# Kernel tuning notes

Hardware: AMD Instinct MI355X
Metric: run time of the kernel (lower is better)

Reference implementation:

```python
import jax, jax.numpy as jnp
import numpy as np

N = 100000
E = 2000000
K = 3


def setup_inputs() -> dict:
    key = jax.random.key(0)
    ks = jax.random.split(key, 6)
    x = jax.random.normal(ks[0], (N, 1), jnp.float32)
    edge_index = jax.random.randint(ks[1], (2, E), 0, N, dtype=jnp.int64)
    W1 = jax.random.normal(ks[2], (K, 1, 32), jnp.float32) * 0.5
    b1 = jnp.zeros((32,), jnp.float32)
    W2 = jax.random.normal(ks[3], (K, 32, 32), jnp.float32) * (1.0 / np.sqrt(32.0))
    b2 = jnp.zeros((32,), jnp.float32)
    Wfc = jax.random.normal(ks[4], (32, 1), jnp.float32) * (1.0 / np.sqrt(32.0))
    bfc = jnp.zeros((1,), jnp.float32)
    return dict(x=x, edge_index=edge_index, W1=W1, b1=b1, W2=W2, b2=b2, Wfc=Wfc, bfc=bfc)


def _cheb_norm(edge_index, n):
    # PyG ChebConv.__norm__ with normalization='sym', lambda_max=2.0:
    # L = I - D^{-1/2} A D^{-1/2}; L_hat = (2/lmax)*L - I = -D^{-1/2} A D^{-1/2} (zero diag)
    src, dst = edge_index[0], edge_index[1]
    w = jnp.ones((edge_index.shape[1],), jnp.float32)
    deg = jax.ops.segment_sum(w, src, num_segments=n)
    dinv = jnp.where(deg > 0, jax.lax.rsqrt(jnp.maximum(deg, 1.0)), 0.0)
    norm = -dinv[src] * w * dinv[dst]
    return src, dst, norm


def _propagate(x, src, dst, norm, n):
    # y[i] = sum_{e: dst[e]=i} norm[e] * x[src[e]]  (gather-scatter SpMM)
    return jax.ops.segment_sum(norm[:, None] * x[src], dst, num_segments=n)


def _cheb_conv(x, src, dst, norm, W, b, n):
    Tx0 = x
    out = Tx0 @ W[0]
    Tx1 = _propagate(Tx0, src, dst, norm, n)
    out = out + Tx1 @ W[1]
    for k in range(2, W.shape[0]):  # small fixed K, structurally distinct weights
        Tx2 = 2.0 * _propagate(Tx1, src, dst, norm, n) - Tx0
        out = out + Tx2 @ W[k]
        Tx0, Tx1 = Tx1, Tx2
    return out + b


def reference(x, edge_index, W1, b1, W2, b2, Wfc, bfc):
    n = x.shape[0]
    src, dst, norm = _cheb_norm(edge_index, n)
    h = jax.nn.relu(_cheb_conv(x, src, dst, norm, W1, b1, n))
    h = jax.nn.relu(_cheb_conv(h, src, dst, norm, W2, b2, n))
    return h @ Wfc + bfc
```

## Files before the change

### kernel.cpp

```cpp
#include <hip/hip_runtime.h>
#include <hip/hip_fp16.h>


#define BS 256
#define NC 32
#define NRH 16
#define NRB 16
#define HB 1024
#define RCAP 6250

__global__ __launch_bounds__(HB) void k_hist32(const int* __restrict__ src,
                                               const int* __restrict__ dst,
                                               int* __restrict__ deg32,
                                               int* __restrict__ cnt32,
                                               int n, int E, int ce) {
    __shared__ int hcnt[RCAP];
    __shared__ int hdeg[RCAP];
    int b = blockIdx.x, c = b & (NC - 1), r = b >> 5;
    int t = threadIdx.x;
    const int R = (n + NRH - 1) / NRH;
    int lo = r * R, hi = min(lo + R, n), len = hi - lo;
    for (int q = t; q < len; q += HB) { hcnt[q] = 0; hdeg[q] = 0; }
    __syncthreads();
    int e0 = c * ce, e1 = min(e0 + ce, E);
    if (e0 < e1) {
        const int4* d4 = reinterpret_cast<const int4*>(dst + e0);
        const int4* s4 = reinterpret_cast<const int4*>(src + e0);
        int L4 = (e1 - e0) >> 2;
        for (int m = 0; m * 4 * HB < L4; ++m) {
            int4 dv[4], sv[4];
            bool ok[4];
            #pragma unroll
            for (int q = 0; q < 4; ++q) {
                int idx = t + (m * 4 + q) * HB;
                ok[q] = idx < L4;
                if (ok[q]) { dv[q] = d4[idx]; sv[q] = s4[idx]; }
            }
            #pragma unroll
            for (int q = 0; q < 4; ++q) if (ok[q]) {
                int d;
                d = dv[q].x; if (d >= lo && d < hi) atomicAdd(&hcnt[d - lo], 1);
                d = dv[q].y; if (d >= lo && d < hi) atomicAdd(&hcnt[d - lo], 1);
                d = dv[q].z; if (d >= lo && d < hi) atomicAdd(&hcnt[d - lo], 1);
                d = dv[q].w; if (d >= lo && d < hi) atomicAdd(&hcnt[d - lo], 1);
                d = sv[q].x; if (d >= lo && d < hi) atomicAdd(&hdeg[d - lo], 1);
                d = sv[q].y; if (d >= lo && d < hi) atomicAdd(&hdeg[d - lo], 1);
                d = sv[q].z; if (d >= lo && d < hi) atomicAdd(&hdeg[d - lo], 1);
                d = sv[q].w; if (d >= lo && d < hi) atomicAdd(&hdeg[d - lo], 1);
            }
        }
        for (int e = e0 + ((e1 - e0) & ~3) + t; e < e1; e += HB) {
            int d = dst[e];
            if (d >= lo && d < hi) atomicAdd(&hcnt[d - lo], 1);
            int s = src[e];
            if (s >= lo && s < hi) atomicAdd(&hdeg[s - lo], 1);
        }
    }
    __syncthreads();
    int base = c * n + lo;
    for (int q = t; q < len; q += HB) {
        cnt32[base + q] = hcnt[q];
        deg32[base + q] = hdeg[q];
    }
}

__global__ void k_dinv32(const int* __restrict__ deg32, const int* __restrict__ cnt32,
                         const float* __restrict__ x, float* __restrict__ dinv,
                         float* __restrict__ u, float* __restrict__ w,
                         int* __restrict__ cnt, int n) {
    int i = blockIdx.x * BS + threadIdx.x;
    if (i < n) {
        int d = 0, ci = 0;
        #pragma unroll
        for (int c = 0; c < NC; ++c) { d += deg32[c * n + i]; ci += cnt32[c * n + i]; }
        float df = (float)d;
        float dv = (d > 0) ? rsqrtf(fmaxf(df, 1.0f)) : 0.0f;
        dinv[i] = dv;
        u[i] = dv * x[i];
        w[i] = -dv * dv;
        cnt[i] = ci;
    }
}

__global__ void k_scan2A(const int* __restrict__ cnt, int* __restrict__ rowptr,
                         int* __restrict__ part, int n) {
    __shared__ int sh[BS];
    int t = threadIdx.x, i = blockIdx.x * BS + t;
    int v = (i < n) ? cnt[i] : 0;
    sh[t] = v; __syncthreads();
    int acc = v;
    for (int d = 1; d < BS; d <<= 1) {
        int add = (t >= d) ? sh[t - d] : 0;
        __syncthreads();
        acc += add; sh[t] = acc;
        __syncthreads();
    }
    if (i < n) rowptr[i] = acc - v;
    if (t == BS - 1) part[blockIdx.x] = acc;
}

__global__ void k_scanB(int* __restrict__ part, int nb) {
    __shared__ int sh[512];
    int t = threadIdx.x;
    int v = (t < nb) ? part[t] : 0;
    sh[t] = v; __syncthreads();
    int acc = v;
    for (int d = 1; d < 512; d <<= 1) {
        int add = (t >= d) ? sh[t - d] : 0;
        __syncthreads();
        acc += add; sh[t] = acc;
        __syncthreads();
    }
    if (t < nb) part[t] = acc - v;
}

__global__ void k_scan2C(int* __restrict__ rowptr, const int* __restrict__ part, int n, int E) {
    int i = blockIdx.x * BS + threadIdx.x;
    if (i < n) rowptr[i] += part[i >> 8];
    if (i == n) rowptr[n] = E;
}

__global__ void k_frag(const int* __restrict__ cnt32, const int* __restrict__ rowptr,
                       int* __restrict__ cur32, int n) {
    int i = blockIdx.x * BS + threadIdx.x;
    if (i < n) {
        int run = rowptr[i];
        #pragma unroll
        for (int c = 0; c < NC; ++c) {
            cur32[c * n + i] = run;
            run += cnt32[c * n + i];
        }
    }
}

__global__ __launch_bounds__(HB) void k_build32(const int* __restrict__ src,
                                                const int* __restrict__ dst,
                                                const int* __restrict__ cur32,
                                                int* __restrict__ colv,
                                                int n, int E, int ce) {
    __shared__ int lcur[RCAP];
    int b = blockIdx.x, r = b & (NRB - 1), c = b >> 4;
    int t = threadIdx.x;
    const int R = (n + NRB - 1) / NRB;
    int lo = r * R, hi = min(lo + R, n), len = hi - lo;
    int base = c * n + lo;
    for (int q = t; q < len; q += HB) lcur[q] = cur32[base + q];
    __syncthreads();
    int e0 = c * ce, e1 = min(e0 + ce, E);
    if (e0 < e1) {
        const int4* d4 = reinterpret_cast<const int4*>(dst + e0);
        const int4* s4 = reinterpret_cast<const int4*>(src + e0);
        int L4 = (e1 - e0) >> 2;
        for (int m = 0; m * 4 * HB < L4; ++m) {
            int4 dv[4], sv[4];
            bool ok[4];
            #pragma unroll
            for (int q = 0; q < 4; ++q) {
                int idx = t + (m * 4 + q) * HB;
                ok[q] = idx < L4;
                if (ok[q]) { dv[q] = d4[idx]; sv[q] = s4[idx]; }
            }
            #pragma unroll
            for (int q = 0; q < 4; ++q) if (ok[q]) {
                int d;
                d = dv[q].x; if (d >= lo && d < hi) { int p = atomicAdd(&lcur[d - lo], 1); colv[p] = sv[q].x; }
                d = dv[q].y; if (d >= lo && d < hi) { int p = atomicAdd(&lcur[d - lo], 1); colv[p] = sv[q].y; }
                d = dv[q].z; if (d >= lo && d < hi) { int p = atomicAdd(&lcur[d - lo], 1); colv[p] = sv[q].z; }
                d = dv[q].w; if (d >= lo && d < hi) { int p = atomicAdd(&lcur[d - lo], 1); colv[p] = sv[q].w; }
            }
        }
        for (int e = e0 + ((e1 - e0) & ~3) + t; e < e1; e += HB) {
            int d = dst[e];
            if (d >= lo && d < hi) { int p = atomicAdd(&lcur[d - lo], 1); colv[p] = src[e]; }
        }
    }
}

__global__ void k_prop_s(const int* __restrict__ rowptr, const int* __restrict__ colv,
                         const float* __restrict__ in, float* __restrict__ g,
                         float* __restrict__ vout, const float* __restrict__ w, int n) {
    int i = blockIdx.x * BS + threadIdx.x;
    if (i >= n) return;
    int b = rowptr[i], e = rowptr[i + 1];
    float s = 0.0f;
    int j = b;
    for (; j + 4 <= e; j += 4) {
        int s0 = colv[j], s1 = colv[j + 1], s2 = colv[j + 2], s3 = colv[j + 3];
        float a0 = in[s0], a1 = in[s1], a2 = in[s2], a3 = in[s3];
        s += (a0 + a1) + (a2 + a3);
    }
    for (; j < e; ++j) s += in[colv[j]];
    g[i] = s;
    if (vout) vout[i] = w[i] * s;
}

__global__ void k_layer1(const float* __restrict__ x, const float* __restrict__ g1,
                         const float* __restrict__ g2, const float* __restrict__ dinv,
                         const float* __restrict__ W1, const float* __restrict__ b1,
                         float* __restrict__ h, __half* __restrict__ hs16, int n) {
    int idx = blockIdx.x * BS + threadIdx.x;
    if (idx < n * 32) {
        int i = idx >> 5, f = idx & 31;
        float x0 = x[i], dv = dinv[i];
        float t1 = -dv * g1[i];
        float t2 = -2.0f * dv * g2[i] - x0;
        float v = x0 * W1[f] + t1 * W1[32 + f] + t2 * W1[64 + f] + b1[f];
        v = fmaxf(v, 0.0f);
        h[idx] = v;
        hs16[idx] = __float2half_rn(dv * v);
    }
}

__global__ void k_prop_vh(const int* __restrict__ rowptr, const int* __restrict__ colv,
                          const __half* __restrict__ in16, float* __restrict__ outf,
                          __half* __restrict__ out16, int n) {
    int t = blockIdx.x * BS + threadIdx.x;
    int node = t >> 3;
    if (node >= n) return;
    int ln4 = (t & 7) << 2;
    int b = rowptr[node], e = rowptr[node + 1];
    float4 acc = make_float4(0.f, 0.f, 0.f, 0.f);
    int j = b;
    for (; j + 8 <= e; j += 8) {
        int sx[8];
        #pragma unroll
        for (int q = 0; q < 8; ++q) sx[q] = colv[j + q];
        float2 raw[8];
        #pragma unroll
        for (int q = 0; q < 8; ++q)
            raw[q] = *reinterpret_cast<const float2*>(in16 + (size_t)sx[q] * 32 + ln4);
        #pragma unroll
        for (int q = 0; q < 8; ++q) {
            __half2 p0 = *reinterpret_cast<__half2*>(&raw[q].x);
            __half2 p1 = *reinterpret_cast<__half2*>(&raw[q].y);
            float2 a = __half22float2(p0), c = __half22float2(p1);
            acc.x += a.x; acc.y += a.y; acc.z += c.x; acc.w += c.y;
        }
    }
    for (; j < e; ++j) {
        int s = colv[j];
        float2 raw = *reinterpret_cast<const float2*>(in16 + (size_t)s * 32 + ln4);
        __half2 p0 = *reinterpret_cast<__half2*>(&raw.x);
        __half2 p1 = *reinterpret_cast<__half2*>(&raw.y);
        float2 a = __half22float2(p0), c = __half22float2(p1);
        acc.x += a.x; acc.y += a.y; acc.z += c.x; acc.w += c.y;
    }
    *reinterpret_cast<float4*>(outf + (size_t)node * 32 + ln4) = acc;
    __half2 o0 = __floats2half2_rn(acc.x, acc.y);
    __half2 o1 = __floats2half2_rn(acc.z, acc.w);
    float2 packed;
    *reinterpret_cast<__half2*>(&packed.x) = o0;
    *reinterpret_cast<__half2*>(&packed.y) = o1;
    *reinterpret_cast<float2*>(out16 + (size_t)node * 32 + ln4) = packed;
}

__global__ __launch_bounds__(BS) void k_prop_fc(
    const int* __restrict__ rowptr, const int* __restrict__ colv,
    const __half* __restrict__ gA16, const float* __restrict__ h,
    const float* __restrict__ gA, const float* __restrict__ wsc,
    const float* __restrict__ dinv, const float* __restrict__ W2,
    const float* __restrict__ b2, const float* __restrict__ Wfc,
    const float* __restrict__ bfc, float* __restrict__ out, int n) {
    __shared__ float W2s[3 * 32 * 32];
    __shared__ float hx[32][33], gax[32][33], gbx[32][33];
    int tid = threadIdx.x;
    for (int q = tid; q < 3 * 32 * 32; q += BS) W2s[q] = W2[q];
    int nd = tid >> 3, ln = tid & 7, ln4 = ln << 2;
    int i = blockIdx.x * 32 + nd;
    float4 acc = make_float4(0.f, 0.f, 0.f, 0.f);
    if (i < n) {
        int b = rowptr[i], e = rowptr[i + 1];
        int j = b;
        for (; j + 8 <= e; j += 8) {
            int sx[8];
            #pragma unroll
            for (int q = 0; q < 8; ++q) sx[q] = colv[j + q];
            float2 raw[8];
            #pragma unroll
            for (int q = 0; q < 8; ++q)
                raw[q] = *reinterpret_cast<const float2*>(gA16 + (size_t)sx[q] * 32 + ln4);
            float mm[8];
            #pragma unroll
            for (int q = 0; q < 8; ++q) mm[q] = wsc[sx[q]];
            #pragma unroll
            for (int q = 0; q < 8; ++q) {
                __half2 p0 = *reinterpret_cast<__half2*>(&raw[q].x);
                __half2 p1 = *reinterpret_cast<__half2*>(&raw[q].y);
                float2 a = __half22float2(p0), c = __half22float2(p1);
                acc.x += mm[q] * a.x; acc.y += mm[q] * a.y;
                acc.z += mm[q] * c.x; acc.w += mm[q] * c.y;
            }
        }
        for (; j < e; ++j) {
            int s = colv[j];
            float m = wsc[s];
            float2 raw = *reinterpret_cast<const float2*>(gA16 + (size_t)s * 32 + ln4);
            __half2 p0 = *reinterpret_cast<__half2*>(&raw.x);
            __half2 p1 = *reinterpret_cast<__half2*>(&raw.y);
            float2 a = __half22float2(p0), c = __half22float2(p1);
            acc.x += m * a.x; acc.y += m * a.y; acc.z += m * c.x; acc.w += m * c.y;
        }
        float4 hv  = *reinterpret_cast<const float4*>(h  + (size_t)i * 32 + ln4);
        float4 gav = *reinterpret_cast<const float4*>(gA + (size_t)i * 32 + ln4);
        hx[nd][ln4 + 0] = hv.x;  hx[nd][ln4 + 1] = hv.y;
        hx[nd][ln4 + 2] = hv.z;  hx[nd][ln4 + 3] = hv.w;
        gax[nd][ln4 + 0] = gav.x; gax[nd][ln4 + 1] = gav.y;
        gax[nd][ln4 + 2] = gav.z; gax[nd][ln4 + 3] = gav.w;
        gbx[nd][ln4 + 0] = acc.x; gbx[nd][ln4 + 1] = acc.y;
        gbx[nd][ln4 + 2] = acc.z; gbx[nd][ln4 + 3] = acc.w;
    }
    __syncthreads();
    if (i < n) {
        float dv = dinv[i];
        float a0 = b2[ln4 + 0], a1 = b2[ln4 + 1], a2 = b2[ln4 + 2], a3 = b2[ln4 + 3];
        #pragma unroll 8
        for (int k = 0; k < 32; ++k) {
            float hk  = hx[nd][k];
            float s1k = -dv * gax[nd][k];
            float s2k = -2.0f * dv * gbx[nd][k] - hk;
            const float* w0 = W2s + k * 32 + ln4;
            a0 += hk * w0[0] + s1k * w0[1024] + s2k * w0[2048];
            a1 += hk * w0[1] + s1k * w0[1025] + s2k * w0[2049];
            a2 += hk * w0[2] + s1k * w0[1026] + s2k * w0[2050];
            a3 += hk * w0[3] + s1k * w0[1027] + s2k * w0[2051];
        }
        float p = fmaxf(a0, 0.f) * Wfc[ln4 + 0] + fmaxf(a1, 0.f) * Wfc[ln4 + 1]
                + fmaxf(a2, 0.f) * Wfc[ln4 + 2] + fmaxf(a3, 0.f) * Wfc[ln4 + 3];
        #pragma unroll
        for (int m = 4; m >= 1; m >>= 1) p += __shfl_xor(p, m, 8);
        if (ln == 0) out[i] = p + bfc[0];
    }
}

extern "C" void kernel_launch(void* const* d_in, const int* in_sizes, int n_in,
                              void* d_out, int out_size, void* d_ws, size_t ws_size,
                              hipStream_t stream) {
    const float* x   = (const float*)d_in[0];
    const int*   ei  = (const int*)d_in[1];
    const float* W1  = (const float*)d_in[2];
    const float* b1  = (const float*)d_in[3];
    const float* W2  = (const float*)d_in[4];
    const float* b2  = (const float*)d_in[5];
    const float* Wfc = (const float*)d_in[6];
    const float* bfc = (const float*)d_in[7];
    float* out = (float*)d_out;

    const int n = in_sizes[0];
    const int E = in_sizes[1] / 2;
    const int* src = ei;
    const int* dst = ei + E;
    const int ce = (((E + NC - 1) / NC) + 3) & ~3;

    int*   cnt    = (int*)d_ws;
    int*   rowptr = cnt + n;
    int*   part   = rowptr + n + 4;
    float* dinv   = (float*)(part + 512);
    float* u      = dinv + n;
    float* w      = u + n;
    float* g1     = w + n;
    float* v1     = g1 + n;
    float* g2     = v1 + n;
    int*   colv   = (int*)(g2 + n);
    float* h      = (float*)(colv + E);
    float* R2     = h + (size_t)32 * n;
    float* gA     = R2 + (size_t)32 * n;
    __half* hs16  = (__half*)R2;
    __half* gA16  = (__half*)(R2 + (size_t)16 * n);
    int*   cnt32  = (int*)h;
    int*   cur32  = (int*)R2;
    int*   deg32  = (int*)gA;

    const int NB = (n + BS - 1) / BS;

    k_hist32<<<NC * NRH, HB, 0, stream>>>(src, dst, deg32, cnt32, n, E, ce);
    k_dinv32<<<NB, BS, 0, stream>>>(deg32, cnt32, x, dinv, u, w, cnt, n);
    k_scan2A<<<NB, BS, 0, stream>>>(cnt, rowptr, part, n);
    k_scanB<<<1, 512, 0, stream>>>(part, NB);
    k_scan2C<<<NB + 1, BS, 0, stream>>>(rowptr, part, n, E);
    k_frag<<<NB, BS, 0, stream>>>(cnt32, rowptr, cur32, n);
    k_build32<<<NC * NRB, HB, 0, stream>>>(src, dst, cur32, colv, n, E, ce);

    k_prop_s<<<NB, BS, 0, stream>>>(rowptr, colv, u, g1, v1, w, n);
    k_prop_s<<<NB, BS, 0, stream>>>(rowptr, colv, v1, g2, nullptr, nullptr, n);
    k_layer1<<<(n * 32 + BS - 1) / BS, BS, 0, stream>>>(x, g1, g2, dinv, W1, b1, h, hs16, n);

    k_prop_vh<<<(n * 8 + BS - 1) / BS, BS, 0, stream>>>(rowptr, colv, hs16, gA, gA16, n);
    k_prop_fc<<<(n + 31) / 32, BS, 0, stream>>>(rowptr, colv, gA16, h, gA, w, dinv,
                                                W2, b2, Wfc, bfc, out, n);
}
```

Before: 275.4 us.

## Prescale fp16 gather source by per-node weight and replace LDS staging with shuffles

k_prop_vh now multiplies its fp16 output by the per-node scale wsc before storing, so k_prop_fc no longer gathers wsc[src] per edge and does a plain sum. The dense 32x96 mixing in k_prop_fc broadcasts the per-node features across the 8-lane group with __shfl instead of staging them in three padded LDS tiles, which removes shared-memory traffic and the mid-kernel barrier. Prescaling before the fp16 rounding slightly changes numerics, and the fully unrolled 32-step loop with 96 shuffles may raise instruction count and register pressure.

```diff
diff --git a/kernel.cpp b/kernel.cpp
--- a/kernel.cpp
+++ b/kernel.cpp
@@ -212,8 +212,8 @@
 }
 
 __global__ void k_prop_vh(const int* __restrict__ rowptr, const int* __restrict__ colv,
-                          const __half* __restrict__ in16, float* __restrict__ outf,
-                          __half* __restrict__ out16, int n) {
+                          const __half* __restrict__ in16, const float* __restrict__ wsc,
+                          float* __restrict__ outf, __half* __restrict__ out16, int n) {
     int t = blockIdx.x * BS + threadIdx.x;
     int node = t >> 3;
     if (node >= n) return;
@@ -246,8 +246,9 @@
         acc.x += a.x; acc.y += a.y; acc.z += c.x; acc.w += c.y;
     }
     *reinterpret_cast<float4*>(outf + (size_t)node * 32 + ln4) = acc;
-    __half2 o0 = __floats2half2_rn(acc.x, acc.y);
-    __half2 o1 = __floats2half2_rn(acc.z, acc.w);
+    float wn = wsc[node];
+    __half2 o0 = __floats2half2_rn(wn * acc.x, wn * acc.y);
+    __half2 o1 = __floats2half2_rn(wn * acc.z, wn * acc.w);
     float2 packed;
     *reinterpret_cast<__half2*>(&packed.x) = o0;
     *reinterpret_cast<__half2*>(&packed.y) = o1;
@@ -256,80 +257,70 @@
 
 __global__ __launch_bounds__(BS) void k_prop_fc(
     const int* __restrict__ rowptr, const int* __restrict__ colv,
-    const __half* __restrict__ gA16, const float* __restrict__ h,
-    const float* __restrict__ gA, const float* __restrict__ wsc,
-    const float* __restrict__ dinv, const float* __restrict__ W2,
-    const float* __restrict__ b2, const float* __restrict__ Wfc,
-    const float* __restrict__ bfc, float* __restrict__ out, int n) {
+    const __half* __restrict__ gA16s, const float* __restrict__ h,
+    const float* __restrict__ gA, const float* __restrict__ dinv,
+    const float* __restrict__ W2, const float* __restrict__ b2,
+    const float* __restrict__ Wfc, const float* __restrict__ bfc,
+    float* __restrict__ out, int n) {
     __shared__ float W2s[3 * 32 * 32];
-    __shared__ float hx[32][33], gax[32][33], gbx[32][33];
     int tid = threadIdx.x;
     for (int q = tid; q < 3 * 32 * 32; q += BS) W2s[q] = W2[q];
+    __syncthreads();
     int nd = tid >> 3, ln = tid & 7, ln4 = ln << 2;
     int i = blockIdx.x * 32 + nd;
+    if (i >= n) return;
     float4 acc = make_float4(0.f, 0.f, 0.f, 0.f);
-    if (i < n) {
-        int b = rowptr[i], e = rowptr[i + 1];
-        int j = b;
-        for (; j + 8 <= e; j += 8) {
-            int sx[8];
-            #pragma unroll
-            for (int q = 0; q < 8; ++q) sx[q] = colv[j + q];
-            float2 raw[8];
-            #pragma unroll
-            for (int q = 0; q < 8; ++q)
-                raw[q] = *reinterpret_cast<const float2*>(gA16 + (size_t)sx[q] * 32 + ln4);
-            float mm[8];
-            #pragma unroll
-            for (int q = 0; q < 8; ++q) mm[q] = wsc[sx[q]];
-            #pragma unroll
-            for (int q = 0; q < 8; ++q) {
-                __half2 p0 = *reinterpret_cast<__half2*>(&raw[q].x);
-                __half2 p1 = *reinterpret_cast<__half2*>(&raw[q].y);
-                float2 a = __half22float2(p0), c = __half22float2(p1);
-                acc.x += mm[q] * a.x; acc.y += mm[q] * a.y;
-                acc.z += mm[q] * c.x; acc.w += mm[q] * c.y;
-            }
-        }
-        for (; j < e; ++j) {
-            int s = colv[j];
-            float m = wsc[s];
-            float2 raw = *reinterpret_cast<const float2*>(gA16 + (size_t)s * 32 + ln4);
-            __half2 p0 = *reinterpret_cast<__half2*>(&raw.x);
-            __half2 p1 = *reinterpret_cast<__half2*>(&raw.y);
+    int b = rowptr[i], e = rowptr[i + 1];
+    int j = b;
+    for (; j + 8 <= e; j += 8) {
+        int sx[8];
+        #pragma unroll
+        for (int q = 0; q < 8; ++q) sx[q] = colv[j + q];
+        float2 raw[8];
+        #pragma unroll
+        for (int q = 0; q < 8; ++q)
+            raw[q] = *reinterpret_cast<const float2*>(gA16s + (size_t)sx[q] * 32 + ln4);
+        #pragma unroll
+        for (int q = 0; q < 8; ++q) {
+            __half2 p0 = *reinterpret_cast<__half2*>(&raw[q].x);
+            __half2 p1 = *reinterpret_cast<__half2*>(&raw[q].y);
             float2 a = __half22float2(p0), c = __half22float2(p1);
-            acc.x += m * a.x; acc.y += m * a.y; acc.z += m * c.x; acc.w += m * c.y;
-        }
-        float4 hv  = *reinterpret_cast<const float4*>(h  + (size_t)i * 32 + ln4);
-        float4 gav = *reinterpret_cast<const float4*>(gA + (size_t)i * 32 + ln4);
-        hx[nd][ln4 + 0] = hv.x;  hx[nd][ln4 + 1] = hv.y;
-        hx[nd][ln4 + 2] = hv.z;  hx[nd][ln4 + 3] = hv.w;
-        gax[nd][ln4 + 0] = gav.x; gax[nd][ln4 + 1] = gav.y;
-        gax[nd][ln4 + 2] = gav.z; gax[nd][ln4 + 3] = gav.w;
-        gbx[nd][ln4 + 0] = acc.x; gbx[nd][ln4 + 1] = acc.y;
-        gbx[nd][ln4 + 2] = acc.z; gbx[nd][ln4 + 3] = acc.w;
-    }
-    __syncthreads();
-    if (i < n) {
-        float dv = dinv[i];
-        float a0 = b2[ln4 + 0], a1 = b2[ln4 + 1], a2 = b2[ln4 + 2], a3 = b2[ln4 + 3];
-        #pragma unroll 8
-        for (int k = 0; k < 32; ++k) {
-            float hk  = hx[nd][k];
-            float s1k = -dv * gax[nd][k];
-            float s2k = -2.0f * dv * gbx[nd][k] - hk;
-            const float* w0 = W2s + k * 32 + ln4;
-            a0 += hk * w0[0] + s1k * w0[1024] + s2k * w0[2048];
-            a1 += hk * w0[1] + s1k * w0[1025] + s2k * w0[2049];
-            a2 += hk * w0[2] + s1k * w0[1026] + s2k * w0[2050];
-            a3 += hk * w0[3] + s1k * w0[1027] + s2k * w0[2051];
-        }
-        float p = fmaxf(a0, 0.f) * Wfc[ln4 + 0] + fmaxf(a1, 0.f) * Wfc[ln4 + 1]
-                + fmaxf(a2, 0.f) * Wfc[ln4 + 2] + fmaxf(a3, 0.f) * Wfc[ln4 + 3];
-        #pragma unroll
-        for (int m = 4; m >= 1; m >>= 1) p += __shfl_xor(p, m, 8);
-        if (ln == 0) out[i] = p + bfc[0];
-    }
+            acc.x += a.x; acc.y += a.y; acc.z += c.x; acc.w += c.y;
+        }
+    }
+    for (; j < e; ++j) {
+        int s = colv[j];
+        float2 raw = *reinterpret_cast<const float2*>(gA16s + (size_t)s * 32 + ln4);
+        __half2 p0 = *reinterpret_cast<__half2*>(&raw.x);
+        __half2 p1 = *reinterpret_cast<__half2*>(&raw.y);
+        float2 a = __half22float2(p0), c = __half22float2(p1);
+        acc.x += a.x; acc.y += a.y; acc.z += c.x; acc.w += c.y;
+    }
+    float dv = dinv[i];
+    float4 hv  = *reinterpret_cast<const float4*>(h  + (size_t)i * 32 + ln4);
+    float4 gav = *reinterpret_cast<const float4*>(gA + (size_t)i * 32 + ln4);
+    float hkv[4] = { hv.x, hv.y, hv.z, hv.w };
+    float s1v[4] = { -dv * gav.x, -dv * gav.y, -dv * gav.z, -dv * gav.w };
+    float s2v[4] = { -2.0f * dv * acc.x - hv.x, -2.0f * dv * acc.y - hv.y,
+                     -2.0f * dv * acc.z - hv.z, -2.0f * dv * acc.w - hv.w };
+    float a0 = b2[ln4 + 0], a1 = b2[ln4 + 1], a2 = b2[ln4 + 2], a3 = b2[ln4 + 3];
+    #pragma unroll
+    for (int k = 0; k < 32; ++k) {
+        int srcLn = k >> 2;
+        float hk  = __shfl(hkv[k & 3], srcLn, 8);
+        float s1k = __shfl(s1v[k & 3], srcLn, 8);
+        float s2k = __shfl(s2v[k & 3], srcLn, 8);
+        const float* w0 = W2s + k * 32 + ln4;
+        a0 += hk * w0[0] + s1k * w0[1024] + s2k * w0[2048];
+        a1 += hk * w0[1] + s1k * w0[1025] + s2k * w0[2049];
+        a2 += hk * w0[2] + s1k * w0[1026] + s2k * w0[2050];
+        a3 += hk * w0[3] + s1k * w0[1027] + s2k * w0[2051];
+    }
+    float p = fmaxf(a0, 0.f) * Wfc[ln4 + 0] + fmaxf(a1, 0.f) * Wfc[ln4 + 1]
+            + fmaxf(a2, 0.f) * Wfc[ln4 + 2] + fmaxf(a3, 0.f) * Wfc[ln4 + 3];
+    #pragma unroll
+    for (int m = 4; m >= 1; m >>= 1) p += __shfl_xor(p, m, 8);
+    if (ln == 0) out[i] = p + bfc[0];
 }
 
 extern "C" void kernel_launch(void* const* d_in, const int* in_sizes, int n_in,
@@ -365,7 +356,7 @@
     float* R2     = h + (size_t)32 * n;
     float* gA     = R2 + (size_t)32 * n;
     __half* hs16  = (__half*)R2;
-    __half* gA16  = (__half*)(R2 + (size_t)16 * n);
+    __half* gA16s = (__half*)(R2 + (size_t)16 * n);
     int*   cnt32  = (int*)h;
     int*   cur32  = (int*)R2;
     int*   deg32  = (int*)gA;
@@ -384,7 +375,7 @@
     k_prop_s<<<NB, BS, 0, stream>>>(rowptr, colv, v1, g2, nullptr, nullptr, n);
     k_layer1<<<(n * 32 + BS - 1) / BS, BS, 0, stream>>>(x, g1, g2, dinv, W1, b1, h, hs16, n);
 
-    k_prop_vh<<<(n * 8 + BS - 1) / BS, BS, 0, stream>>>(rowptr, colv, hs16, gA, gA16, n);
-    k_prop_fc<<<(n + 31) / 32, BS, 0, stream>>>(rowptr, colv, gA16, h, gA, w, dinv,
+    k_prop_vh<<<(n * 8 + BS - 1) / BS, BS, 0, stream>>>(rowptr, colv, hs16, w, gA, gA16s, n);
+    k_prop_fc<<<(n + 31) / 32, BS, 0, stream>>>(rowptr, colv, gA16s, h, gA, dinv,
                                                 W2, b2, Wfc, bfc, out, n);
 }
```

New measurement: 271.8 us. Within noise of the previous version (-1.3%).
